# Optimization experiments

Hardware: AMD Instinct MI355X
Metric: run time of the kernel (lower is better)

Reference implementation:

```python
import jax, jax.numpy as jnp
from jax import lax
import numpy as np

H = 32  # hidden size
I = 1   # input size

def setup_inputs() -> dict:
    key = jax.random.key(0)
    ks = jax.random.split(key, 8)
    B, T = 4096, 512
    s_ih = 1.0 / np.sqrt(H)
    inp = {
        "x": jax.random.normal(ks[0], (B, T, I), dtype=jnp.float32),
        # PyTorch LSTM params, gate order (i, f, g, o)
        "W_ih": jax.random.uniform(ks[1], (4 * H, I), dtype=jnp.float32, minval=-s_ih, maxval=s_ih),
        "W_hh": jax.random.uniform(ks[2], (4 * H, H), dtype=jnp.float32, minval=-s_ih, maxval=s_ih),
        "b_ih": jax.random.uniform(ks[3], (4 * H,), dtype=jnp.float32, minval=-s_ih, maxval=s_ih),
        "b_hh": jax.random.uniform(ks[4], (4 * H,), dtype=jnp.float32, minval=-s_ih, maxval=s_ih),
        "W_head": jax.random.uniform(ks[5], (1, H), dtype=jnp.float32, minval=-s_ih, maxval=s_ih),
        "b_head": jax.random.uniform(ks[6], (1,), dtype=jnp.float32, minval=-s_ih, maxval=s_ih),
    }
    return inp

def reference(x, W_ih, W_hh, b_ih, b_hh, W_head, b_head):
    B, T, _ = x.shape
    # Precompute input contribution to all gates: [B, T, 4H]
    x_gates = jnp.einsum('bti,gi->btg', x, W_ih) + b_ih + b_hh

    def step(carry, xg_t):  # xg_t: [B, 4H]
        h, c = carry
        gates = xg_t + h @ W_hh.T
        i, f, g, o = jnp.split(gates, 4, axis=-1)
        i = jax.nn.sigmoid(i)
        f = jax.nn.sigmoid(f)
        g = jnp.tanh(g)
        o = jax.nn.sigmoid(o)
        c = f * c + i * g
        h = o * jnp.tanh(c)
        return (h, c), None

    h0 = jnp.zeros((B, H), dtype=x.dtype)
    c0 = jnp.zeros((B, H), dtype=x.dtype)
    (h_last, _), _ = lax.scan(step, (h0, c0), jnp.swapaxes(x_gates, 0, 1))
    # head on last timestep: [B, 1]
    return h_last @ W_head.T + b_head
```

## Files before the change

### kernel.cpp

```cpp
#include <hip/hip_runtime.h>

#define HID 32
#define SEQ 512
#define WAVES_PER_BLOCK 4
#define BLOCK (WAVES_PER_BLOCK * 64)

typedef float v2f __attribute__((ext_vector_type(2)));


#define PKP(IFE, IFO, GOE, GOO, HP) \
  "v_pk_fma_f32 v[80:81], v[" IFE "], v[" HP "], v[80:81] op_sel_hi:[1,0,1]\n\t" \
  "v_pk_fma_f32 v[82:83], v[" GOE "], v[" HP "], v[82:83] op_sel_hi:[1,0,1]\n\t" \
  "v_pk_fma_f32 v[80:81], v[" IFO "], v[" HP "], v[80:81] op_sel:[0,1,0] op_sel_hi:[1,1,1]\n\t" \
  "v_pk_fma_f32 v[82:83], v[" GOO "], v[" HP "], v[82:83] op_sel:[0,1,0] op_sel_hi:[1,1,1]\n\t"

#define STEP(TT) \
  "ds_read2_b32 v[84:85], %[xa] offset0:" TT " offset1:" TT "\n\t" \
  "ds_read_b128 v[64:67], %[hr] offset:0\n\t" \
  "ds_read_b128 v[68:71], %[hr] offset:16\n\t" \
  "ds_read_b128 v[72:75], %[hr] offset:32\n\t" \
  "ds_read_b128 v[76:79], %[hr] offset:48\n\t" \
  "s_waitcnt lgkmcnt(4)\n\t" \
  "v_pk_fma_f32 v[80:81], %[uvIF], v[84:85], %[bvIF]\n\t" \
  "v_pk_fma_f32 v[82:83], %[uvGO], v[84:85], %[bvGO]\n\t" \
  "s_waitcnt lgkmcnt(3)\n\t" \
  PKP("96:97","98:99","160:161","162:163","64:65") \
  PKP("100:101","102:103","164:165","166:167","66:67") \
  "ds_read_b128 v[64:67], %[hr] offset:64\n\t" \
  "s_waitcnt lgkmcnt(3)\n\t" \
  PKP("104:105","106:107","168:169","170:171","68:69") \
  PKP("108:109","110:111","172:173","174:175","70:71") \
  "ds_read_b128 v[68:71], %[hr] offset:80\n\t" \
  "s_waitcnt lgkmcnt(3)\n\t" \
  PKP("112:113","114:115","176:177","178:179","72:73") \
  PKP("116:117","118:119","180:181","182:183","74:75") \
  "ds_read_b128 v[72:75], %[hr] offset:96\n\t" \
  "s_waitcnt lgkmcnt(3)\n\t" \
  PKP("120:121","122:123","184:185","186:187","76:77") \
  PKP("124:125","126:127","188:189","190:191","78:79") \
  "ds_read_b128 v[76:79], %[hr] offset:112\n\t" \
  "s_waitcnt lgkmcnt(3)\n\t" \
  PKP("128:129","130:131","192:193","194:195","64:65") \
  PKP("132:133","134:135","196:197","198:199","66:67") \
  "s_waitcnt lgkmcnt(2)\n\t" \
  PKP("136:137","138:139","200:201","202:203","68:69") \
  PKP("140:141","142:143","204:205","206:207","70:71") \
  "s_waitcnt lgkmcnt(1)\n\t" \
  PKP("144:145","146:147","208:209","210:211","72:73") \
  PKP("148:149","150:151","212:213","214:215","74:75") \
  "s_waitcnt lgkmcnt(0)\n\t" \
  PKP("152:153","154:155","216:217","218:219","76:77") \
  PKP("156:157","158:159","220:221","222:223","78:79") \
  "v_mul_f32 v86, 0xbfb8aa3b, v80\n\t" \
  "v_mul_f32 v87, 0xbfb8aa3b, v81\n\t" \
  "v_mul_f32 v88, 0x4038aa3b, v82\n\t" \
  "v_mul_f32 v89, 0xbfb8aa3b, v83\n\t" \
  "v_exp_f32 v86, v86\n\t" \
  "v_exp_f32 v87, v87\n\t" \
  "v_exp_f32 v88, v88\n\t" \
  "v_exp_f32 v89, v89\n\t" \
  "v_add_f32 v86, 1.0, v86\n\t" \
  "v_add_f32 v87, 1.0, v87\n\t" \
  "v_add_f32 v88, 1.0, v88\n\t" \
  "v_add_f32 v89, 1.0, v89\n\t" \
  "v_rcp_f32 v86, v86\n\t" \
  "v_rcp_f32 v87, v87\n\t" \
  "v_rcp_f32 v88, v88\n\t" \
  "v_rcp_f32 v89, v89\n\t" \
  "s_nop 1\n\t" \
  "v_fma_f32 v90, -2.0, v88, 1.0\n\t" \
  "v_mul_f32 v91, v86, v90\n\t" \
  "v_fma_f32 %[c], v87, %[c], v91\n\t" \
  "v_mul_f32 v92, 0x4038aa3b, %[c]\n\t" \
  "v_exp_f32 v92, v92\n\t" \
  "s_nop 1\n\t" \
  "v_add_f32 v92, 1.0, v92\n\t" \
  "v_rcp_f32 v92, v92\n\t" \
  "s_nop 1\n\t" \
  "v_fma_f32 v92, -2.0, v92, 1.0\n\t" \
  "v_mul_f32 %[h], v89, v92\n\t" \
  "ds_write_b32 %[hw], %[h]\n\t"

#define CLOBS \
  "v64","v65","v66","v67","v68","v69","v70","v71","v72","v73","v74","v75", \
  "v76","v77","v78","v79","v80","v81","v82","v83","v84","v85","v86","v87", \
  "v88","v89","v90","v91","v92","v93","v94","v95","v96","v97","v98","v99", \
  "v100","v101","v102","v103","v104","v105","v106","v107","v108","v109", \
  "v110","v111","v112","v113","v114","v115","v116","v117","v118","v119", \
  "v120","v121","v122","v123","v124","v125","v126","v127","v128","v129", \
  "v130","v131","v132","v133","v134","v135","v136","v137","v138","v139", \
  "v140","v141","v142","v143","v144","v145","v146","v147","v148","v149", \
  "v150","v151","v152","v153","v154","v155","v156","v157","v158","v159", \
  "v160","v161","v162","v163","v164","v165","v166","v167","v168","v169", \
  "v170","v171","v172","v173","v174","v175","v176","v177","v178","v179", \
  "v180","v181","v182","v183","v184","v185","v186","v187","v188","v189", \
  "v190","v191","v192","v193","v194","v195","v196","v197","v198","v199", \
  "v200","v201","v202","v203","v204","v205","v206","v207","v208","v209", \
  "v210","v211","v212","v213","v214","v215","v216","v217","v218","v219", \
  "v220","v221","v222","v223"

__global__ __launch_bounds__(BLOCK)
void lstm_fused_kernel(
    const float* __restrict__ x,
    const float* __restrict__ W_ih,
    const float* __restrict__ W_hh,
    const float* __restrict__ b_ih,
    const float* __restrict__ b_hh,
    const float* __restrict__ W_head,
    const float* __restrict__ b_head,
    float* __restrict__ out)
{
    __shared__ __align__(16) v2f WIFL[32][34];
    __shared__ __align__(16) v2f WGOL[32][34];
    __shared__ __align__(16) float Hbuf[WAVES_PER_BLOCK][2][32];
    __shared__ __align__(16) float Xbuf[WAVES_PER_BLOCK][2][32];

    const int tid = threadIdx.x;
    for (int idx = tid; idx < 1024; idx += BLOCK) {
        const int u = idx >> 5;
        const int j = idx & 31;
        WIFL[u][j] = (v2f){ W_hh[u * 32 + j],        W_hh[(32 + u) * 32 + j] };
        WGOL[u][j] = (v2f){ W_hh[(64 + u) * 32 + j], W_hh[(96 + u) * 32 + j] };
    }
    __syncthreads();

    const int lane = tid & 63;
    const int u    = lane & 31;
    const int s    = lane >> 5;
    const int wid  = tid >> 6;
    const int b0   = 2 * (blockIdx.x * WAVES_PER_BLOCK + wid);

    {
        const unsigned aIF = (unsigned)(size_t)&WIFL[u][0];
        const unsigned aGO = (unsigned)(size_t)&WGOL[u][0];
        asm volatile(
            "ds_read_b128 v[96:99],   %[wa] offset:0\n\t"
            "ds_read_b128 v[100:103], %[wa] offset:16\n\t"
            "ds_read_b128 v[104:107], %[wa] offset:32\n\t"
            "ds_read_b128 v[108:111], %[wa] offset:48\n\t"
            "ds_read_b128 v[112:115], %[wa] offset:64\n\t"
            "ds_read_b128 v[116:119], %[wa] offset:80\n\t"
            "ds_read_b128 v[120:123], %[wa] offset:96\n\t"
            "ds_read_b128 v[124:127], %[wa] offset:112\n\t"
            "ds_read_b128 v[128:131], %[wa] offset:128\n\t"
            "ds_read_b128 v[132:135], %[wa] offset:144\n\t"
            "ds_read_b128 v[136:139], %[wa] offset:160\n\t"
            "ds_read_b128 v[140:143], %[wa] offset:176\n\t"
            "ds_read_b128 v[144:147], %[wa] offset:192\n\t"
            "ds_read_b128 v[148:151], %[wa] offset:208\n\t"
            "ds_read_b128 v[152:155], %[wa] offset:224\n\t"
            "ds_read_b128 v[156:159], %[wa] offset:240\n\t"
            "ds_read_b128 v[160:163], %[wb] offset:0\n\t"
            "ds_read_b128 v[164:167], %[wb] offset:16\n\t"
            "ds_read_b128 v[168:171], %[wb] offset:32\n\t"
            "ds_read_b128 v[172:175], %[wb] offset:48\n\t"
            "ds_read_b128 v[176:179], %[wb] offset:64\n\t"
            "ds_read_b128 v[180:183], %[wb] offset:80\n\t"
            "ds_read_b128 v[184:187], %[wb] offset:96\n\t"
            "ds_read_b128 v[188:191], %[wb] offset:112\n\t"
            "ds_read_b128 v[192:195], %[wb] offset:128\n\t"
            "ds_read_b128 v[196:199], %[wb] offset:144\n\t"
            "ds_read_b128 v[200:203], %[wb] offset:160\n\t"
            "ds_read_b128 v[204:207], %[wb] offset:176\n\t"
            "ds_read_b128 v[208:211], %[wb] offset:192\n\t"
            "ds_read_b128 v[212:215], %[wb] offset:208\n\t"
            "ds_read_b128 v[216:219], %[wb] offset:224\n\t"
            "ds_read_b128 v[220:223], %[wb] offset:240\n\t"
            "s_waitcnt lgkmcnt(0)"
            :
            : [wa]"v"(aIF), [wb]"v"(aGO)
            : "memory", CLOBS);
    }

    const v2f bvIF = { b_ih[u]      + b_hh[u],      b_ih[32 + u] + b_hh[32 + u] };
    const v2f bvGO = { b_ih[64 + u] + b_hh[64 + u], b_ih[96 + u] + b_hh[96 + u] };
    const v2f uvIF = { W_ih[u],      W_ih[32 + u] };
    const v2f uvGO = { W_ih[64 + u], W_ih[96 + u] };

    const unsigned hr = (unsigned)(size_t)&Hbuf[wid][s][0];
    const unsigned hw = hr + (unsigned)(u * 4);
    const unsigned xa = (unsigned)(size_t)&Xbuf[wid][s][0];

    const float* xb = x + (size_t)(b0 + s) * SEQ;

    float h = 0.0f, c = 0.0f;
    Hbuf[wid][s][u] = 0.0f;

#pragma unroll 1
    for (int t0 = 0; t0 < SEQ; t0 += 32) {
        Xbuf[wid][s][u] = xb[t0 + u];
        asm volatile(
            STEP("0")  STEP("1")  STEP("2")  STEP("3")
            STEP("4")  STEP("5")  STEP("6")  STEP("7")
            STEP("8")  STEP("9")  STEP("10") STEP("11")
            STEP("12") STEP("13") STEP("14") STEP("15")
            STEP("16") STEP("17") STEP("18") STEP("19")
            STEP("20") STEP("21") STEP("22") STEP("23")
            STEP("24") STEP("25") STEP("26") STEP("27")
            STEP("28") STEP("29") STEP("30") STEP("31")
            : [h]"+v"(h), [c]"+v"(c)
            : [hr]"v"(hr), [hw]"v"(hw), [xa]"v"(xa),
              [uvIF]"v"(uvIF), [bvIF]"v"(bvIF),
              [uvGO]"v"(uvGO), [bvGO]"v"(bvGO)
            : "memory", CLOBS);
    }

    float v = h * W_head[u];
#pragma unroll
    for (int off = 16; off >= 1; off >>= 1)
        v += __shfl_xor(v, off);
    if (u == 0) out[b0 + s] = v + b_head[0];
}

extern "C" void kernel_launch(void* const* d_in, const int* in_sizes, int n_in,
                              void* d_out, int out_size, void* d_ws, size_t ws_size,
                              hipStream_t stream) {
    const float* x      = (const float*)d_in[0];
    const float* W_ih   = (const float*)d_in[1];
    const float* W_hh   = (const float*)d_in[2];
    const float* b_ih   = (const float*)d_in[3];
    const float* b_hh   = (const float*)d_in[4];
    const float* W_head = (const float*)d_in[5];
    const float* b_head = (const float*)d_in[6];
    float* out = (float*)d_out;

    const int B = in_sizes[0] / SEQ;
    const int grid = B / (2 * WAVES_PER_BLOCK);

    lstm_fused_kernel<<<grid, BLOCK, 0, stream>>>(
        x, W_ih, W_hh, b_ih, b_hh, W_head, b_head, out);
}
```

Baseline: 295.1 us.

## Interleave two independent LSTM sample streams per wave to hide activation latency

Each wave now carries two independent groups of samples (A and B), four samples per wave instead of two. The matvec of one group is software-pipelined against the sigmoid/tanh chain of the other, so transcendental and LDS latency in the serial recurrence is overlapped. The whole x sequence for the block is preloaded into LDS once, replacing the per-32-step global loads, and the grid is halved. The cost is about 256 VGPRs, which limits occupancy, plus a larger LDS footprint and much more complex hand-written asm.

```diff
diff --git a/kernel.cpp b/kernel.cpp
--- a/kernel.cpp
+++ b/kernel.cpp
@@ -8,78 +8,145 @@
 typedef float v2f __attribute__((ext_vector_type(2)));
 
 
-#define PKP(IFE, IFO, GOE, GOO, HP) \
-  "v_pk_fma_f32 v[80:81], v[" IFE "], v[" HP "], v[80:81] op_sel_hi:[1,0,1]\n\t" \
-  "v_pk_fma_f32 v[82:83], v[" GOE "], v[" HP "], v[82:83] op_sel_hi:[1,0,1]\n\t" \
-  "v_pk_fma_f32 v[80:81], v[" IFO "], v[" HP "], v[80:81] op_sel:[0,1,0] op_sel_hi:[1,1,1]\n\t" \
-  "v_pk_fma_f32 v[82:83], v[" GOO "], v[" HP "], v[82:83] op_sel:[0,1,0] op_sel_hi:[1,1,1]\n\t"
-
-#define STEP(TT) \
-  "ds_read2_b32 v[84:85], %[xa] offset0:" TT " offset1:" TT "\n\t" \
-  "ds_read_b128 v[64:67], %[hr] offset:0\n\t" \
-  "ds_read_b128 v[68:71], %[hr] offset:16\n\t" \
-  "ds_read_b128 v[72:75], %[hr] offset:32\n\t" \
-  "ds_read_b128 v[76:79], %[hr] offset:48\n\t" \
+#define GRP(AIF, AGO, WA, WB, WC, WD, HP) \
+  "v_pk_fma_f32 v[" AIF "], v[" WA "], v[" HP "], v[" AIF "] op_sel_hi:[1,0,1]\n\t" \
+  "v_pk_fma_f32 v[" AGO "], v[" WC "], v[" HP "], v[" AGO "] op_sel_hi:[1,0,1]\n\t" \
+  "v_pk_fma_f32 v[" AIF "], v[" WB "], v[" HP "], v[" AIF "] op_sel:[0,1,0] op_sel_hi:[1,1,1]\n\t" \
+  "v_pk_fma_f32 v[" AGO "], v[" WD "], v[" HP "], v[" AGO "] op_sel:[0,1,0] op_sel_hi:[1,1,1]\n\t"
+
+#define SLOT(XIF,XGO, XQ0,XQ1,XQ2,XQ3, XP0,XP1,XP2,XP3,XP4,XP5,XP6,XP7, XXP, XXA, XHR, \
+             YI,YF,YG,YO, YU0,YU1,YU2,YU3,YU4,YU5,YU6, YC,YH, YHW, YXP, YXA, YHR, YQ0,YQ1,YQ2,YQ3) \
+  "v_mul_f32 v" YU0 ", 0xbfb8aa3b, v" YI "\n\t" \
+  "v_mul_f32 v" YU1 ", 0xbfb8aa3b, v" YF "\n\t" \
+  "v_exp_f32 v" YU0 ", v" YU0 "\n\t" \
+  "v_exp_f32 v" YU1 ", v" YU1 "\n\t" \
+  "v_mul_f32 v" YU2 ", 0x4038aa3b, v" YG "\n\t" \
+  "v_mul_f32 v" YU3 ", 0xbfb8aa3b, v" YO "\n\t" \
+  "v_exp_f32 v" YU2 ", v" YU2 "\n\t" \
+  "v_exp_f32 v" YU3 ", v" YU3 "\n\t" \
+  "s_waitcnt lgkmcnt(4)\n\t" \
+  "v_pk_fma_f32 v[" XIF "], %[uvIF], v[" XXP "], %[bvIF]\n\t" \
+  "v_pk_fma_f32 v[" XGO "], %[uvGO], v[" XXP "], %[bvGO]\n\t" \
+  "v_add_u32 " XXA ", 4, " XXA "\n\t" \
+  "s_waitcnt lgkmcnt(3)\n\t" \
+  GRP(XIF,XGO,"128:129","130:131","192:193","194:195",XP0) \
+  GRP(XIF,XGO,"132:133","134:135","196:197","198:199",XP1) \
+  "v_add_f32 v" YU0 ", 1.0, v" YU0 "\n\t" \
+  "v_add_f32 v" YU1 ", 1.0, v" YU1 "\n\t" \
+  "ds_read_b128 v[" XQ0 "], " XHR " offset:64\n\t" \
+  "s_waitcnt lgkmcnt(3)\n\t" \
+  GRP(XIF,XGO,"136:137","138:139","200:201","202:203",XP2) \
+  GRP(XIF,XGO,"140:141","142:143","204:205","206:207",XP3) \
+  "v_add_f32 v" YU2 ", 1.0, v" YU2 "\n\t" \
+  "v_add_f32 v" YU3 ", 1.0, v" YU3 "\n\t" \
+  "ds_read_b128 v[" XQ1 "], " XHR " offset:80\n\t" \
+  "s_waitcnt lgkmcnt(3)\n\t" \
+  GRP(XIF,XGO,"144:145","146:147","208:209","210:211",XP4) \
+  GRP(XIF,XGO,"148:149","150:151","212:213","214:215",XP5) \
+  "v_rcp_f32 v" YU0 ", v" YU0 "\n\t" \
+  "v_rcp_f32 v" YU1 ", v" YU1 "\n\t" \
+  "ds_read_b128 v[" XQ2 "], " XHR " offset:96\n\t" \
+  "s_waitcnt lgkmcnt(3)\n\t" \
+  GRP(XIF,XGO,"152:153","154:155","216:217","218:219",XP6) \
+  GRP(XIF,XGO,"156:157","158:159","220:221","222:223",XP7) \
+  "v_rcp_f32 v" YU2 ", v" YU2 "\n\t" \
+  "v_rcp_f32 v" YU3 ", v" YU3 "\n\t" \
+  "ds_read_b128 v[" XQ3 "], " XHR " offset:112\n\t" \
+  "s_waitcnt lgkmcnt(3)\n\t" \
+  GRP(XIF,XGO,"160:161","162:163","224:225","226:227",XP0) \
+  GRP(XIF,XGO,"164:165","166:167","228:229","230:231",XP1) \
+  "v_fma_f32 v" YU4 ", -2.0, v" YU2 ", 1.0\n\t" \
+  "v_mul_f32 v" YU5 ", v" YU0 ", v" YU4 "\n\t" \
+  "s_waitcnt lgkmcnt(2)\n\t" \
+  GRP(XIF,XGO,"168:169","170:171","232:233","234:235",XP2) \
+  GRP(XIF,XGO,"172:173","174:175","236:237","238:239",XP3) \
+  "v_fma_f32 " YC ", v" YU1 ", " YC ", v" YU5 "\n\t" \
+  "v_mul_f32 v" YU6 ", 0x4038aa3b, " YC "\n\t" \
+  "s_waitcnt lgkmcnt(1)\n\t" \
+  GRP(XIF,XGO,"176:177","178:179","240:241","242:243",XP4) \
+  GRP(XIF,XGO,"180:181","182:183","244:245","246:247",XP5) \
+  "v_exp_f32 v" YU6 ", v" YU6 "\n\t" \
+  "s_waitcnt lgkmcnt(0)\n\t" \
+  GRP(XIF,XGO,"184:185","186:187","248:249","250:251",XP6) \
+  "v_add_f32 v" YU6 ", 1.0, v" YU6 "\n\t" \
+  "v_rcp_f32 v" YU6 ", v" YU6 "\n\t" \
+  GRP(XIF,XGO,"188:189","190:191","252:253","254:255",XP7) \
+  "v_fma_f32 v" YU6 ", -2.0, v" YU6 ", 1.0\n\t" \
+  "v_mul_f32 " YH ", v" YU3 ", v" YU6 "\n\t" \
+  "ds_write_b32 " YHW ", " YH "\n\t" \
+  "ds_read2_b32 v[" YXP "], " YXA " offset0:0 offset1:0\n\t" \
+  "ds_read_b128 v[" YQ0 "], " YHR " offset:0\n\t" \
+  "ds_read_b128 v[" YQ1 "], " YHR " offset:16\n\t" \
+  "ds_read_b128 v[" YQ2 "], " YHR " offset:32\n\t" \
+  "ds_read_b128 v[" YQ3 "], " YHR " offset:48\n\t"
+
+#define SLOTX(...) SLOT(__VA_ARGS__)
+
+#define PROMAC \
   "s_waitcnt lgkmcnt(4)\n\t" \
   "v_pk_fma_f32 v[80:81], %[uvIF], v[84:85], %[bvIF]\n\t" \
   "v_pk_fma_f32 v[82:83], %[uvGO], v[84:85], %[bvGO]\n\t" \
-  "s_waitcnt lgkmcnt(3)\n\t" \
-  PKP("96:97","98:99","160:161","162:163","64:65") \
-  PKP("100:101","102:103","164:165","166:167","66:67") \
-  "ds_read_b128 v[64:67], %[hr] offset:64\n\t" \
-  "s_waitcnt lgkmcnt(3)\n\t" \
-  PKP("104:105","106:107","168:169","170:171","68:69") \
-  PKP("108:109","110:111","172:173","174:175","70:71") \
-  "ds_read_b128 v[68:71], %[hr] offset:80\n\t" \
-  "s_waitcnt lgkmcnt(3)\n\t" \
-  PKP("112:113","114:115","176:177","178:179","72:73") \
-  PKP("116:117","118:119","180:181","182:183","74:75") \
-  "ds_read_b128 v[72:75], %[hr] offset:96\n\t" \
-  "s_waitcnt lgkmcnt(3)\n\t" \
-  PKP("120:121","122:123","184:185","186:187","76:77") \
-  PKP("124:125","126:127","188:189","190:191","78:79") \
-  "ds_read_b128 v[76:79], %[hr] offset:112\n\t" \
-  "s_waitcnt lgkmcnt(3)\n\t" \
-  PKP("128:129","130:131","192:193","194:195","64:65") \
-  PKP("132:133","134:135","196:197","198:199","66:67") \
+  "v_add_u32 %[xaA], 4, %[xaA]\n\t" \
+  "s_waitcnt lgkmcnt(3)\n\t" \
+  GRP("80:81","82:83","128:129","130:131","192:193","194:195","64:65") \
+  GRP("80:81","82:83","132:133","134:135","196:197","198:199","66:67") \
+  "ds_read_b128 v[64:67], %[hrA] offset:64\n\t" \
+  "s_waitcnt lgkmcnt(3)\n\t" \
+  GRP("80:81","82:83","136:137","138:139","200:201","202:203","68:69") \
+  GRP("80:81","82:83","140:141","142:143","204:205","206:207","70:71") \
+  "ds_read_b128 v[68:71], %[hrA] offset:80\n\t" \
+  "s_waitcnt lgkmcnt(3)\n\t" \
+  GRP("80:81","82:83","144:145","146:147","208:209","210:211","72:73") \
+  GRP("80:81","82:83","148:149","150:151","212:213","214:215","74:75") \
+  "ds_read_b128 v[72:75], %[hrA] offset:96\n\t" \
+  "s_waitcnt lgkmcnt(3)\n\t" \
+  GRP("80:81","82:83","152:153","154:155","216:217","218:219","76:77") \
+  GRP("80:81","82:83","156:157","158:159","220:221","222:223","78:79") \
+  "ds_read_b128 v[76:79], %[hrA] offset:112\n\t" \
+  "s_waitcnt lgkmcnt(3)\n\t" \
+  GRP("80:81","82:83","160:161","162:163","224:225","226:227","64:65") \
+  GRP("80:81","82:83","164:165","166:167","228:229","230:231","66:67") \
   "s_waitcnt lgkmcnt(2)\n\t" \
-  PKP("136:137","138:139","200:201","202:203","68:69") \
-  PKP("140:141","142:143","204:205","206:207","70:71") \
+  GRP("80:81","82:83","168:169","170:171","232:233","234:235","68:69") \
+  GRP("80:81","82:83","172:173","174:175","236:237","238:239","70:71") \
   "s_waitcnt lgkmcnt(1)\n\t" \
-  PKP("144:145","146:147","208:209","210:211","72:73") \
-  PKP("148:149","150:151","212:213","214:215","74:75") \
+  GRP("80:81","82:83","176:177","178:179","240:241","242:243","72:73") \
+  GRP("80:81","82:83","180:181","182:183","244:245","246:247","74:75") \
   "s_waitcnt lgkmcnt(0)\n\t" \
-  PKP("152:153","154:155","216:217","218:219","76:77") \
-  PKP("156:157","158:159","220:221","222:223","78:79") \
-  "v_mul_f32 v86, 0xbfb8aa3b, v80\n\t" \
-  "v_mul_f32 v87, 0xbfb8aa3b, v81\n\t" \
-  "v_mul_f32 v88, 0x4038aa3b, v82\n\t" \
-  "v_mul_f32 v89, 0xbfb8aa3b, v83\n\t" \
-  "v_exp_f32 v86, v86\n\t" \
-  "v_exp_f32 v87, v87\n\t" \
-  "v_exp_f32 v88, v88\n\t" \
-  "v_exp_f32 v89, v89\n\t" \
-  "v_add_f32 v86, 1.0, v86\n\t" \
-  "v_add_f32 v87, 1.0, v87\n\t" \
-  "v_add_f32 v88, 1.0, v88\n\t" \
-  "v_add_f32 v89, 1.0, v89\n\t" \
-  "v_rcp_f32 v86, v86\n\t" \
-  "v_rcp_f32 v87, v87\n\t" \
-  "v_rcp_f32 v88, v88\n\t" \
-  "v_rcp_f32 v89, v89\n\t" \
+  GRP("80:81","82:83","184:185","186:187","248:249","250:251","76:77") \
+  GRP("80:81","82:83","188:189","190:191","252:253","254:255","78:79")
+
+#define PLAINACT(YI,YF,YG,YO, YU0,YU1,YU2,YU3,YU4,YU5,YU6, YC,YH,YHW) \
+  "v_mul_f32 v" YU0 ", 0xbfb8aa3b, v" YI "\n\t" \
+  "v_mul_f32 v" YU1 ", 0xbfb8aa3b, v" YF "\n\t" \
+  "v_mul_f32 v" YU2 ", 0x4038aa3b, v" YG "\n\t" \
+  "v_mul_f32 v" YU3 ", 0xbfb8aa3b, v" YO "\n\t" \
+  "v_exp_f32 v" YU0 ", v" YU0 "\n\t" \
+  "v_exp_f32 v" YU1 ", v" YU1 "\n\t" \
+  "v_exp_f32 v" YU2 ", v" YU2 "\n\t" \
+  "v_exp_f32 v" YU3 ", v" YU3 "\n\t" \
   "s_nop 1\n\t" \
-  "v_fma_f32 v90, -2.0, v88, 1.0\n\t" \
-  "v_mul_f32 v91, v86, v90\n\t" \
-  "v_fma_f32 %[c], v87, %[c], v91\n\t" \
-  "v_mul_f32 v92, 0x4038aa3b, %[c]\n\t" \
-  "v_exp_f32 v92, v92\n\t" \
+  "v_add_f32 v" YU0 ", 1.0, v" YU0 "\n\t" \
+  "v_add_f32 v" YU1 ", 1.0, v" YU1 "\n\t" \
+  "v_add_f32 v" YU2 ", 1.0, v" YU2 "\n\t" \
+  "v_add_f32 v" YU3 ", 1.0, v" YU3 "\n\t" \
+  "v_rcp_f32 v" YU0 ", v" YU0 "\n\t" \
+  "v_rcp_f32 v" YU1 ", v" YU1 "\n\t" \
+  "v_rcp_f32 v" YU2 ", v" YU2 "\n\t" \
+  "v_rcp_f32 v" YU3 ", v" YU3 "\n\t" \
   "s_nop 1\n\t" \
-  "v_add_f32 v92, 1.0, v92\n\t" \
-  "v_rcp_f32 v92, v92\n\t" \
+  "v_fma_f32 v" YU4 ", -2.0, v" YU2 ", 1.0\n\t" \
+  "v_mul_f32 v" YU5 ", v" YU0 ", v" YU4 "\n\t" \
+  "v_fma_f32 " YC ", v" YU1 ", " YC ", v" YU5 "\n\t" \
+  "v_mul_f32 v" YU6 ", 0x4038aa3b, " YC "\n\t" \
+  "v_exp_f32 v" YU6 ", v" YU6 "\n\t" \
   "s_nop 1\n\t" \
-  "v_fma_f32 v92, -2.0, v92, 1.0\n\t" \
-  "v_mul_f32 %[h], v89, v92\n\t" \
-  "ds_write_b32 %[hw], %[h]\n\t"
+  "v_add_f32 v" YU6 ", 1.0, v" YU6 "\n\t" \
+  "v_rcp_f32 v" YU6 ", v" YU6 "\n\t" \
+  "s_nop 1\n\t" \
+  "v_fma_f32 v" YU6 ", -2.0, v" YU6 ", 1.0\n\t" \
+  "v_mul_f32 " YH ", v" YU3 ", v" YU6 "\n\t" \
+  "ds_write_b32 " YHW ", " YH "\n\t"
 
 #define CLOBS \
   "v64","v65","v66","v67","v68","v69","v70","v71","v72","v73","v74","v75", \
@@ -97,7 +164,23 @@
   "v190","v191","v192","v193","v194","v195","v196","v197","v198","v199", \
   "v200","v201","v202","v203","v204","v205","v206","v207","v208","v209", \
   "v210","v211","v212","v213","v214","v215","v216","v217","v218","v219", \
-  "v220","v221","v222","v223"
+  "v220","v221","v222","v223","v224","v225","v226","v227","v228","v229", \
+  "v230","v231","v232","v233","v234","v235","v236","v237","v238","v239", \
+  "v240","v241","v242","v243","v244","v245","v246","v247","v248","v249", \
+  "v250","v251","v252","v253","v254","v255"
+
+#define XA_ARGS "80:81","82:83", "64:67","68:71","72:75","76:79", \
+  "64:65","66:67","68:69","70:71","72:73","74:75","76:77","78:79", \
+  "84:85", "%[xaA]", "%[hrA]"
+#define XB_ARGS "112:113","114:115", "96:99","100:103","104:107","108:111", \
+  "96:97","98:99","100:101","102:103","104:105","106:107","108:109","110:111", \
+  "116:117", "%[xaB]", "%[hrB]"
+#define YA_ARGS "80","81","82","83", "86","87","88","89","90","91","92", \
+  "%[cA]","%[hA]", "%[hwA]", "84:85", "%[xaA]", "%[hrA]", \
+  "64:67","68:71","72:75","76:79"
+#define YB_ARGS "112","113","114","115", "118","119","120","121","122","123","124", \
+  "%[cB]","%[hB]", "%[hwB]", "116:117", "%[xaB]", "%[hrB]", \
+  "96:99","100:103","104:107","108:111"
 
 __global__ __launch_bounds__(BLOCK)
 void lstm_fused_kernel(
@@ -112,8 +195,8 @@
 {
     __shared__ __align__(16) v2f WIFL[32][34];
     __shared__ __align__(16) v2f WGOL[32][34];
-    __shared__ __align__(16) float Hbuf[WAVES_PER_BLOCK][2][32];
-    __shared__ __align__(16) float Xbuf[WAVES_PER_BLOCK][2][32];
+    __shared__ __align__(16) float Xall[WAVES_PER_BLOCK][4][SEQ];
+    __shared__ __align__(16) float Hbuf[WAVES_PER_BLOCK][4][32];
 
     const int tid = threadIdx.x;
     for (int idx = tid; idx < 1024; idx += BLOCK) {
@@ -122,50 +205,58 @@
         WIFL[u][j] = (v2f){ W_hh[u * 32 + j],        W_hh[(32 + u) * 32 + j] };
         WGOL[u][j] = (v2f){ W_hh[(64 + u) * 32 + j], W_hh[(96 + u) * 32 + j] };
     }
+    {
+        const int base = blockIdx.x * 16;
+        for (int idx = tid; idx < 16 * SEQ; idx += BLOCK) {
+            const int smp = idx >> 9;
+            const int t   = idx & (SEQ - 1);
+            Xall[smp >> 2][smp & 3][t] = x[(size_t)(base + smp) * SEQ + t];
+        }
+    }
     __syncthreads();
 
     const int lane = tid & 63;
     const int u    = lane & 31;
     const int s    = lane >> 5;
     const int wid  = tid >> 6;
-    const int b0   = 2 * (blockIdx.x * WAVES_PER_BLOCK + wid);
+    const int bbase = blockIdx.x * 16 + wid * 4;
 
     {
         const unsigned aIF = (unsigned)(size_t)&WIFL[u][0];
         const unsigned aGO = (unsigned)(size_t)&WGOL[u][0];
         asm volatile(
-            "ds_read_b128 v[96:99],   %[wa] offset:0\n\t"
-            "ds_read_b128 v[100:103], %[wa] offset:16\n\t"
-            "ds_read_b128 v[104:107], %[wa] offset:32\n\t"
-            "ds_read_b128 v[108:111], %[wa] offset:48\n\t"
-            "ds_read_b128 v[112:115], %[wa] offset:64\n\t"
-            "ds_read_b128 v[116:119], %[wa] offset:80\n\t"
-            "ds_read_b128 v[120:123], %[wa] offset:96\n\t"
-            "ds_read_b128 v[124:127], %[wa] offset:112\n\t"
-            "ds_read_b128 v[128:131], %[wa] offset:128\n\t"
-            "ds_read_b128 v[132:135], %[wa] offset:144\n\t"
-            "ds_read_b128 v[136:139], %[wa] offset:160\n\t"
-            "ds_read_b128 v[140:143], %[wa] offset:176\n\t"
-            "ds_read_b128 v[144:147], %[wa] offset:192\n\t"
-            "ds_read_b128 v[148:151], %[wa] offset:208\n\t"
-            "ds_read_b128 v[152:155], %[wa] offset:224\n\t"
-            "ds_read_b128 v[156:159], %[wa] offset:240\n\t"
-            "ds_read_b128 v[160:163], %[wb] offset:0\n\t"
-            "ds_read_b128 v[164:167], %[wb] offset:16\n\t"
-            "ds_read_b128 v[168:171], %[wb] offset:32\n\t"
-            "ds_read_b128 v[172:175], %[wb] offset:48\n\t"
-            "ds_read_b128 v[176:179], %[wb] offset:64\n\t"
-            "ds_read_b128 v[180:183], %[wb] offset:80\n\t"
-            "ds_read_b128 v[184:187], %[wb] offset:96\n\t"
-            "ds_read_b128 v[188:191], %[wb] offset:112\n\t"
-            "ds_read_b128 v[192:195], %[wb] offset:128\n\t"
-            "ds_read_b128 v[196:199], %[wb] offset:144\n\t"
-            "ds_read_b128 v[200:203], %[wb] offset:160\n\t"
-            "ds_read_b128 v[204:207], %[wb] offset:176\n\t"
-            "ds_read_b128 v[208:211], %[wb] offset:192\n\t"
-            "ds_read_b128 v[212:215], %[wb] offset:208\n\t"
-            "ds_read_b128 v[216:219], %[wb] offset:224\n\t"
-            "ds_read_b128 v[220:223], %[wb] offset:240\n\t"
+            "ds_read_b128 v[128:131], %[wa] offset:0\n\t"
+            "ds_read_b128 v[132:135], %[wa] offset:16\n\t"
+            "ds_read_b128 v[136:139], %[wa] offset:32\n\t"
+            "ds_read_b128 v[140:143], %[wa] offset:48\n\t"
+            "ds_read_b128 v[144:147], %[wa] offset:64\n\t"
+            "ds_read_b128 v[148:151], %[wa] offset:80\n\t"
+            "ds_read_b128 v[152:155], %[wa] offset:96\n\t"
+            "ds_read_b128 v[156:159], %[wa] offset:112\n\t"
+            "ds_read_b128 v[160:163], %[wa] offset:128\n\t"
+            "ds_read_b128 v[164:167], %[wa] offset:144\n\t"
+            "ds_read_b128 v[168:171], %[wa] offset:160\n\t"
+            "ds_read_b128 v[172:175], %[wa] offset:176\n\t"
+            "ds_read_b128 v[176:179], %[wa] offset:192\n\t"
+            "ds_read_b128 v[180:183], %[wa] offset:208\n\t"
+            "ds_read_b128 v[184:187], %[wa] offset:224\n\t"
+            "ds_read_b128 v[188:191], %[wa] offset:240\n\t"
+            "ds_read_b128 v[192:195], %[wb] offset:0\n\t"
+            "ds_read_b128 v[196:199], %[wb] offset:16\n\t"
+            "ds_read_b128 v[200:203], %[wb] offset:32\n\t"
+            "ds_read_b128 v[204:207], %[wb] offset:48\n\t"
+            "ds_read_b128 v[208:211], %[wb] offset:64\n\t"
+            "ds_read_b128 v[212:215], %[wb] offset:80\n\t"
+            "ds_read_b128 v[216:219], %[wb] offset:96\n\t"
+            "ds_read_b128 v[220:223], %[wb] offset:112\n\t"
+            "ds_read_b128 v[224:227], %[wb] offset:128\n\t"
+            "ds_read_b128 v[228:231], %[wb] offset:144\n\t"
+            "ds_read_b128 v[232:235], %[wb] offset:160\n\t"
+            "ds_read_b128 v[236:239], %[wb] offset:176\n\t"
+            "ds_read_b128 v[240:243], %[wb] offset:192\n\t"
+            "ds_read_b128 v[244:247], %[wb] offset:208\n\t"
+            "ds_read_b128 v[248:251], %[wb] offset:224\n\t"
+            "ds_read_b128 v[252:255], %[wb] offset:240\n\t"
             "s_waitcnt lgkmcnt(0)"
             :
             : [wa]"v"(aIF), [wb]"v"(aGO)
@@ -177,39 +268,68 @@
     const v2f uvIF = { W_ih[u],      W_ih[32 + u] };
     const v2f uvGO = { W_ih[64 + u], W_ih[96 + u] };
 
-    const unsigned hr = (unsigned)(size_t)&Hbuf[wid][s][0];
-    const unsigned hw = hr + (unsigned)(u * 4);
-    const unsigned xa = (unsigned)(size_t)&Xbuf[wid][s][0];
-
-    const float* xb = x + (size_t)(b0 + s) * SEQ;
-
-    float h = 0.0f, c = 0.0f;
-    Hbuf[wid][s][u] = 0.0f;
+    const unsigned hrA = (unsigned)(size_t)&Hbuf[wid][s][0];
+    const unsigned hwA = hrA + (unsigned)(u * 4);
+    const unsigned hrB = (unsigned)(size_t)&Hbuf[wid][2 + s][0];
+    const unsigned hwB = hrB + (unsigned)(u * 4);
+    unsigned xaA = (unsigned)(size_t)&Xall[wid][s][0];
+    unsigned xaB = (unsigned)(size_t)&Xall[wid][2 + s][0];
+
+    float hA = 0.0f, cA = 0.0f, hB = 0.0f, cB = 0.0f;
+    Hbuf[wid][s][u]     = 0.0f;
+    Hbuf[wid][2 + s][u] = 0.0f;
+
+    asm volatile(
+        "ds_read2_b32 v[84:85], %[xaA] offset0:0 offset1:0\n\t"
+        "ds_read_b128 v[64:67], %[hrA] offset:0\n\t"
+        "ds_read_b128 v[68:71], %[hrA] offset:16\n\t"
+        "ds_read_b128 v[72:75], %[hrA] offset:32\n\t"
+        "ds_read_b128 v[76:79], %[hrA] offset:48\n\t"
+        PROMAC
+        "ds_read2_b32 v[116:117], %[xaB] offset0:0 offset1:0\n\t"
+        "ds_read_b128 v[96:99],   %[hrB] offset:0\n\t"
+        "ds_read_b128 v[100:103], %[hrB] offset:16\n\t"
+        "ds_read_b128 v[104:107], %[hrB] offset:32\n\t"
+        "ds_read_b128 v[108:111], %[hrB] offset:48\n\t"
+        : [xaA]"+v"(xaA), [xaB]"+v"(xaB)
+        : [hrA]"v"(hrA), [hrB]"v"(hrB),
+          [uvIF]"v"(uvIF), [bvIF]"v"(bvIF), [uvGO]"v"(uvGO), [bvGO]"v"(bvGO)
+        : "memory", CLOBS);
 
 #pragma unroll 1
-    for (int t0 = 0; t0 < SEQ; t0 += 32) {
-        Xbuf[wid][s][u] = xb[t0 + u];
+    for (int t = 0; t < SEQ - 1; ++t) {
         asm volatile(
-            STEP("0")  STEP("1")  STEP("2")  STEP("3")
-            STEP("4")  STEP("5")  STEP("6")  STEP("7")
-            STEP("8")  STEP("9")  STEP("10") STEP("11")
-            STEP("12") STEP("13") STEP("14") STEP("15")
-            STEP("16") STEP("17") STEP("18") STEP("19")
-            STEP("20") STEP("21") STEP("22") STEP("23")
-            STEP("24") STEP("25") STEP("26") STEP("27")
-            STEP("28") STEP("29") STEP("30") STEP("31")
-            : [h]"+v"(h), [c]"+v"(c)
-            : [hr]"v"(hr), [hw]"v"(hw), [xa]"v"(xa),
-              [uvIF]"v"(uvIF), [bvIF]"v"(bvIF),
-              [uvGO]"v"(uvGO), [bvGO]"v"(bvGO)
+            SLOTX(XB_ARGS, YA_ARGS)
+            SLOTX(XA_ARGS, YB_ARGS)
+            : [hA]"+v"(hA), [cA]"+v"(cA), [hB]"+v"(hB), [cB]"+v"(cB),
+              [xaA]"+v"(xaA), [xaB]"+v"(xaB)
+            : [hrA]"v"(hrA), [hrB]"v"(hrB), [hwA]"v"(hwA), [hwB]"v"(hwB),
+              [uvIF]"v"(uvIF), [bvIF]"v"(bvIF), [uvGO]"v"(uvGO), [bvGO]"v"(bvGO)
             : "memory", CLOBS);
     }
 
-    float v = h * W_head[u];
+    asm volatile(
+        SLOTX(XB_ARGS, YA_ARGS)
+        PLAINACT("112","113","114","115", "118","119","120","121","122","123","124",
+                 "%[cB]","%[hB]","%[hwB]")
+        "s_waitcnt lgkmcnt(0)"
+        : [hA]"+v"(hA), [cA]"+v"(cA), [hB]"+v"(hB), [cB]"+v"(cB),
+          [xaA]"+v"(xaA), [xaB]"+v"(xaB)
+        : [hrA]"v"(hrA), [hrB]"v"(hrB), [hwA]"v"(hwA), [hwB]"v"(hwB),
+          [uvIF]"v"(uvIF), [bvIF]"v"(bvIF), [uvGO]"v"(uvGO), [bvGO]"v"(bvGO)
+        : "memory", CLOBS);
+
+    float vA = hA * W_head[u];
+    float vB = hB * W_head[u];
 #pragma unroll
-    for (int off = 16; off >= 1; off >>= 1)
-        v += __shfl_xor(v, off);
-    if (u == 0) out[b0 + s] = v + b_head[0];
+    for (int off = 16; off >= 1; off >>= 1) {
+        vA += __shfl_xor(vA, off);
+        vB += __shfl_xor(vB, off);
+    }
+    if (u == 0) {
+        out[bbase + s]     = vA + b_head[0];
+        out[bbase + 2 + s] = vB + b_head[0];
+    }
 }
 
 extern "C" void kernel_launch(void* const* d_in, const int* in_sizes, int n_in,
@@ -225,7 +345,7 @@
     float* out = (float*)d_out;
 
     const int B = in_sizes[0] / SEQ;
-    const int grid = B / (2 * WAVES_PER_BLOCK);
+    const int grid = B / 16;
 
     lstm_fused_kernel<<<grid, BLOCK, 0, stream>>>(
         x, W_ih, W_hh, b_ih, b_hh, W_head, b_head, out);
```

Measured after the change: 340.5 us. 15.4% more time.

## Split LSTM step into MAC and activation phases, phase-shifted across wave halves

Applied to the files above, without the earlier changes.

Blocks grow to 8 waves, and each step is split into a matrix-multiply phase and an activation phase, separated by block barriers. Waves 0-3 and 4-7 run these phases offset by one half-step, so MAC-heavy and transcendental-heavy work from different waves should interleave on the SIMDs. The whole x sequence for the block's 16 samples is preloaded into LDS once instead of reloaded per 32-step chunk. The cost is two s_barrier per timestep and more LDS, and breaking the fully unrolled asm into separate blocks gives up the static schedule across steps.

```diff
diff --git a/kernel.cpp b/kernel.cpp
--- a/kernel.cpp
+++ b/kernel.cpp
@@ -2,84 +2,17 @@
 
 #define HID 32
 #define SEQ 512
-#define WAVES_PER_BLOCK 4
+#define WAVES_PER_BLOCK 8
 #define BLOCK (WAVES_PER_BLOCK * 64)
 
 typedef float v2f __attribute__((ext_vector_type(2)));
 
 
-#define PKP(IFE, IFO, GOE, GOO, HP) \
-  "v_pk_fma_f32 v[80:81], v[" IFE "], v[" HP "], v[80:81] op_sel_hi:[1,0,1]\n\t" \
-  "v_pk_fma_f32 v[82:83], v[" GOE "], v[" HP "], v[82:83] op_sel_hi:[1,0,1]\n\t" \
-  "v_pk_fma_f32 v[80:81], v[" IFO "], v[" HP "], v[80:81] op_sel:[0,1,0] op_sel_hi:[1,1,1]\n\t" \
-  "v_pk_fma_f32 v[82:83], v[" GOO "], v[" HP "], v[82:83] op_sel:[0,1,0] op_sel_hi:[1,1,1]\n\t"
-
-#define STEP(TT) \
-  "ds_read2_b32 v[84:85], %[xa] offset0:" TT " offset1:" TT "\n\t" \
-  "ds_read_b128 v[64:67], %[hr] offset:0\n\t" \
-  "ds_read_b128 v[68:71], %[hr] offset:16\n\t" \
-  "ds_read_b128 v[72:75], %[hr] offset:32\n\t" \
-  "ds_read_b128 v[76:79], %[hr] offset:48\n\t" \
-  "s_waitcnt lgkmcnt(4)\n\t" \
-  "v_pk_fma_f32 v[80:81], %[uvIF], v[84:85], %[bvIF]\n\t" \
-  "v_pk_fma_f32 v[82:83], %[uvGO], v[84:85], %[bvGO]\n\t" \
-  "s_waitcnt lgkmcnt(3)\n\t" \
-  PKP("96:97","98:99","160:161","162:163","64:65") \
-  PKP("100:101","102:103","164:165","166:167","66:67") \
-  "ds_read_b128 v[64:67], %[hr] offset:64\n\t" \
-  "s_waitcnt lgkmcnt(3)\n\t" \
-  PKP("104:105","106:107","168:169","170:171","68:69") \
-  PKP("108:109","110:111","172:173","174:175","70:71") \
-  "ds_read_b128 v[68:71], %[hr] offset:80\n\t" \
-  "s_waitcnt lgkmcnt(3)\n\t" \
-  PKP("112:113","114:115","176:177","178:179","72:73") \
-  PKP("116:117","118:119","180:181","182:183","74:75") \
-  "ds_read_b128 v[72:75], %[hr] offset:96\n\t" \
-  "s_waitcnt lgkmcnt(3)\n\t" \
-  PKP("120:121","122:123","184:185","186:187","76:77") \
-  PKP("124:125","126:127","188:189","190:191","78:79") \
-  "ds_read_b128 v[76:79], %[hr] offset:112\n\t" \
-  "s_waitcnt lgkmcnt(3)\n\t" \
-  PKP("128:129","130:131","192:193","194:195","64:65") \
-  PKP("132:133","134:135","196:197","198:199","66:67") \
-  "s_waitcnt lgkmcnt(2)\n\t" \
-  PKP("136:137","138:139","200:201","202:203","68:69") \
-  PKP("140:141","142:143","204:205","206:207","70:71") \
-  "s_waitcnt lgkmcnt(1)\n\t" \
-  PKP("144:145","146:147","208:209","210:211","72:73") \
-  PKP("148:149","150:151","212:213","214:215","74:75") \
-  "s_waitcnt lgkmcnt(0)\n\t" \
-  PKP("152:153","154:155","216:217","218:219","76:77") \
-  PKP("156:157","158:159","220:221","222:223","78:79") \
-  "v_mul_f32 v86, 0xbfb8aa3b, v80\n\t" \
-  "v_mul_f32 v87, 0xbfb8aa3b, v81\n\t" \
-  "v_mul_f32 v88, 0x4038aa3b, v82\n\t" \
-  "v_mul_f32 v89, 0xbfb8aa3b, v83\n\t" \
-  "v_exp_f32 v86, v86\n\t" \
-  "v_exp_f32 v87, v87\n\t" \
-  "v_exp_f32 v88, v88\n\t" \
-  "v_exp_f32 v89, v89\n\t" \
-  "v_add_f32 v86, 1.0, v86\n\t" \
-  "v_add_f32 v87, 1.0, v87\n\t" \
-  "v_add_f32 v88, 1.0, v88\n\t" \
-  "v_add_f32 v89, 1.0, v89\n\t" \
-  "v_rcp_f32 v86, v86\n\t" \
-  "v_rcp_f32 v87, v87\n\t" \
-  "v_rcp_f32 v88, v88\n\t" \
-  "v_rcp_f32 v89, v89\n\t" \
-  "s_nop 1\n\t" \
-  "v_fma_f32 v90, -2.0, v88, 1.0\n\t" \
-  "v_mul_f32 v91, v86, v90\n\t" \
-  "v_fma_f32 %[c], v87, %[c], v91\n\t" \
-  "v_mul_f32 v92, 0x4038aa3b, %[c]\n\t" \
-  "v_exp_f32 v92, v92\n\t" \
-  "s_nop 1\n\t" \
-  "v_add_f32 v92, 1.0, v92\n\t" \
-  "v_rcp_f32 v92, v92\n\t" \
-  "s_nop 1\n\t" \
-  "v_fma_f32 v92, -2.0, v92, 1.0\n\t" \
-  "v_mul_f32 %[h], v89, v92\n\t" \
-  "ds_write_b32 %[hw], %[h]\n\t"
+#define GRP(WA, WB, WC, WD, HP) \
+  "v_pk_fma_f32 v[80:81], v[" WA "], " HP ", v[80:81] op_sel_hi:[1,0,1]\n\t" \
+  "v_pk_fma_f32 v[82:83], v[" WC "], " HP ", v[82:83] op_sel_hi:[1,0,1]\n\t" \
+  "v_pk_fma_f32 v[80:81], v[" WB "], " HP ", v[80:81] op_sel:[0,1,0] op_sel_hi:[1,1,1]\n\t" \
+  "v_pk_fma_f32 v[82:83], v[" WD "], " HP ", v[82:83] op_sel:[0,1,0] op_sel_hi:[1,1,1]\n\t"
 
 #define CLOBS \
   "v64","v65","v66","v67","v68","v69","v70","v71","v72","v73","v74","v75", \
@@ -97,7 +30,89 @@
   "v190","v191","v192","v193","v194","v195","v196","v197","v198","v199", \
   "v200","v201","v202","v203","v204","v205","v206","v207","v208","v209", \
   "v210","v211","v212","v213","v214","v215","v216","v217","v218","v219", \
-  "v220","v221","v222","v223"
+  "v220","v221","v222","v223","v224","v225","v226","v227","v228","v229", \
+  "v230","v231","v232","v233","v234","v235","v236","v237","v238","v239"
+
+#define MAC_ASM(XA) \
+    asm volatile( \
+        "ds_read2_b32 v[84:85], %[xa] offset0:0 offset1:0\n\t" \
+        "ds_read_b128 v[64:67],   %[hr] offset:0\n\t" \
+        "ds_read_b128 v[68:71],   %[hr] offset:16\n\t" \
+        "ds_read_b128 v[72:75],   %[hr] offset:32\n\t" \
+        "ds_read_b128 v[76:79],   %[hr] offset:48\n\t" \
+        "ds_read_b128 v[224:227], %[hr] offset:64\n\t" \
+        "ds_read_b128 v[228:231], %[hr] offset:80\n\t" \
+        "ds_read_b128 v[232:235], %[hr] offset:96\n\t" \
+        "ds_read_b128 v[236:239], %[hr] offset:112\n\t" \
+        "v_add_u32 %[xa], 4, %[xa]\n\t" \
+        "s_waitcnt lgkmcnt(8)\n\t" \
+        "v_pk_fma_f32 v[80:81], %[uvIF], v[84:85], %[bvIF]\n\t" \
+        "v_pk_fma_f32 v[82:83], %[uvGO], v[84:85], %[bvGO]\n\t" \
+        "s_waitcnt lgkmcnt(7)\n\t" \
+        GRP("96:97","98:99","160:161","162:163","v[64:65]") \
+        GRP("100:101","102:103","164:165","166:167","v[66:67]") \
+        "s_waitcnt lgkmcnt(6)\n\t" \
+        GRP("104:105","106:107","168:169","170:171","v[68:69]") \
+        GRP("108:109","110:111","172:173","174:175","v[70:71]") \
+        "s_waitcnt lgkmcnt(5)\n\t" \
+        GRP("112:113","114:115","176:177","178:179","v[72:73]") \
+        GRP("116:117","118:119","180:181","182:183","v[74:75]") \
+        "s_waitcnt lgkmcnt(4)\n\t" \
+        GRP("120:121","122:123","184:185","186:187","v[76:77]") \
+        GRP("124:125","126:127","188:189","190:191","v[78:79]") \
+        "s_waitcnt lgkmcnt(3)\n\t" \
+        GRP("128:129","130:131","192:193","194:195","v[224:225]") \
+        GRP("132:133","134:135","196:197","198:199","v[226:227]") \
+        "s_waitcnt lgkmcnt(2)\n\t" \
+        GRP("136:137","138:139","200:201","202:203","v[228:229]") \
+        GRP("140:141","142:143","204:205","206:207","v[230:231]") \
+        "s_waitcnt lgkmcnt(1)\n\t" \
+        GRP("144:145","146:147","208:209","210:211","v[232:233]") \
+        GRP("148:149","150:151","212:213","214:215","v[234:235]") \
+        "s_waitcnt lgkmcnt(0)\n\t" \
+        GRP("152:153","154:155","216:217","218:219","v[236:237]") \
+        GRP("156:157","158:159","220:221","222:223","v[238:239]") \
+        : [xa]"+v"(XA) \
+        : [hr]"v"(hr), [uvIF]"v"(uvIF), [bvIF]"v"(bvIF), \
+          [uvGO]"v"(uvGO), [bvGO]"v"(bvGO) \
+        : "memory", CLOBS)
+
+#define ACT_ASM() \
+    asm volatile( \
+        "v_mul_f32 v86, 0xbfb8aa3b, v80\n\t" \
+        "v_mul_f32 v87, 0xbfb8aa3b, v81\n\t" \
+        "v_mul_f32 v88, 0x4038aa3b, v82\n\t" \
+        "v_mul_f32 v89, 0xbfb8aa3b, v83\n\t" \
+        "v_exp_f32 v86, v86\n\t" \
+        "v_exp_f32 v87, v87\n\t" \
+        "v_exp_f32 v88, v88\n\t" \
+        "v_exp_f32 v89, v89\n\t" \
+        "v_add_f32 v86, 1.0, v86\n\t" \
+        "v_add_f32 v87, 1.0, v87\n\t" \
+        "v_add_f32 v88, 1.0, v88\n\t" \
+        "v_add_f32 v89, 1.0, v89\n\t" \
+        "v_rcp_f32 v86, v86\n\t" \
+        "v_rcp_f32 v87, v87\n\t" \
+        "v_rcp_f32 v88, v88\n\t" \
+        "v_rcp_f32 v89, v89\n\t" \
+        "s_nop 1\n\t" \
+        "v_fma_f32 v90, -2.0, v88, 1.0\n\t" \
+        "v_mul_f32 v91, v86, v90\n\t" \
+        "v_fma_f32 %[c], v87, %[c], v91\n\t" \
+        "v_mul_f32 v92, 0x4038aa3b, %[c]\n\t" \
+        "v_exp_f32 v92, v92\n\t" \
+        "s_nop 1\n\t" \
+        "v_add_f32 v92, 1.0, v92\n\t" \
+        "v_rcp_f32 v92, v92\n\t" \
+        "s_nop 1\n\t" \
+        "v_fma_f32 v92, -2.0, v92, 1.0\n\t" \
+        "v_mul_f32 %[h], v89, v92\n\t" \
+        "ds_write_b32 %[hw], %[h]\n\t" \
+        : [h]"+v"(h), [c]"+v"(c) \
+        : [hw]"v"(hw) \
+        : "memory", CLOBS)
+
+#define BAR() __builtin_amdgcn_s_barrier()
 
 __global__ __launch_bounds__(BLOCK)
 void lstm_fused_kernel(
@@ -112,8 +127,8 @@
 {
     __shared__ __align__(16) v2f WIFL[32][34];
     __shared__ __align__(16) v2f WGOL[32][34];
+    __shared__ __align__(16) float Xall[WAVES_PER_BLOCK][2][SEQ];
     __shared__ __align__(16) float Hbuf[WAVES_PER_BLOCK][2][32];
-    __shared__ __align__(16) float Xbuf[WAVES_PER_BLOCK][2][32];
 
     const int tid = threadIdx.x;
     for (int idx = tid; idx < 1024; idx += BLOCK) {
@@ -122,13 +137,21 @@
         WIFL[u][j] = (v2f){ W_hh[u * 32 + j],        W_hh[(32 + u) * 32 + j] };
         WGOL[u][j] = (v2f){ W_hh[(64 + u) * 32 + j], W_hh[(96 + u) * 32 + j] };
     }
+    {
+        const int base = blockIdx.x * 16;
+        for (int idx = tid; idx < 16 * SEQ; idx += BLOCK) {
+            const int smp = idx >> 9;
+            const int t   = idx & (SEQ - 1);
+            Xall[smp >> 1][smp & 1][t] = x[(size_t)(base + smp) * SEQ + t];
+        }
+    }
     __syncthreads();
 
     const int lane = tid & 63;
     const int u    = lane & 31;
     const int s    = lane >> 5;
     const int wid  = tid >> 6;
-    const int b0   = 2 * (blockIdx.x * WAVES_PER_BLOCK + wid);
+    const bool even = (wid < 4);
 
     {
         const unsigned aIF = (unsigned)(size_t)&WIFL[u][0];
@@ -179,37 +202,36 @@
 
     const unsigned hr = (unsigned)(size_t)&Hbuf[wid][s][0];
     const unsigned hw = hr + (unsigned)(u * 4);
-    const unsigned xa = (unsigned)(size_t)&Xbuf[wid][s][0];
-
-    const float* xb = x + (size_t)(b0 + s) * SEQ;
+    unsigned xa = (unsigned)(size_t)&Xall[wid][s][0];
 
     float h = 0.0f, c = 0.0f;
     Hbuf[wid][s][u] = 0.0f;
-
+    __syncthreads();
+
+    if (even) {
+        BAR();
 #pragma unroll 1
-    for (int t0 = 0; t0 < SEQ; t0 += 32) {
-        Xbuf[wid][s][u] = xb[t0 + u];
-        asm volatile(
-            STEP("0")  STEP("1")  STEP("2")  STEP("3")
-            STEP("4")  STEP("5")  STEP("6")  STEP("7")
-            STEP("8")  STEP("9")  STEP("10") STEP("11")
-            STEP("12") STEP("13") STEP("14") STEP("15")
-            STEP("16") STEP("17") STEP("18") STEP("19")
-            STEP("20") STEP("21") STEP("22") STEP("23")
-            STEP("24") STEP("25") STEP("26") STEP("27")
-            STEP("28") STEP("29") STEP("30") STEP("31")
-            : [h]"+v"(h), [c]"+v"(c)
-            : [hr]"v"(hr), [hw]"v"(hw), [xa]"v"(xa),
-              [uvIF]"v"(uvIF), [bvIF]"v"(bvIF),
-              [uvGO]"v"(uvGO), [bvGO]"v"(bvGO)
-            : "memory", CLOBS);
+        for (int t = 0; t < SEQ - 1; ++t) {
+            MAC_ASM(xa);  BAR();
+            ACT_ASM();    BAR();
+        }
+        MAC_ASM(xa);  BAR();
+        ACT_ASM();
+    } else {
+        MAC_ASM(xa);  BAR();
+#pragma unroll 1
+        for (int t = 0; t < SEQ - 1; ++t) {
+            ACT_ASM();    BAR();
+            MAC_ASM(xa);  BAR();
+        }
+        ACT_ASM();  BAR();
     }
 
     float v = h * W_head[u];
 #pragma unroll
     for (int off = 16; off >= 1; off >>= 1)
         v += __shfl_xor(v, off);
-    if (u == 0) out[b0 + s] = v + b_head[0];
+    if (u == 0) out[blockIdx.x * 16 + wid * 2 + s] = v + b_head[0];
 }
 
 extern "C" void kernel_launch(void* const* d_in, const int* in_sizes, int n_in,
@@ -225,7 +247,7 @@
     float* out = (float*)d_out;
 
     const int B = in_sizes[0] / SEQ;
-    const int grid = B / (2 * WAVES_PER_BLOCK);
+    const int grid = B / 16;
 
     lstm_fused_kernel<<<grid, BLOCK, 0, stream>>>(
         x, W_ih, W_hh, b_ih, b_hh, W_head, b_head, out);
```

New measurement: 316.2 us. 1.07x slower.
